# Kernel optimization log

Measured on AMD Instinct MI355X. Metric: run time of the kernel, lower is better.

Reference implementation:

```python
import jax, jax.numpy as jnp
import numpy as np

HEADS = 8
GROUPS = 32   # Group_cnt in the source
WIN = 16      # config.local_window_size


def _gn_nc(x, groups, eps):
    # group_norm on [N, C] (affine=False)
    N, C = x.shape
    xg = x.reshape(N, groups, C // groups)
    m = xg.mean(axis=2, keepdims=True)
    v = xg.var(axis=2, keepdims=True)
    return ((xg - m) / jnp.sqrt(v + eps)).reshape(N, C)


def _gn_nchw(x, groups, eps):
    # group_norm on [B, C, H, W] (affine=False)
    B, C, H, W = x.shape
    xg = x.reshape(B, groups, C // groups, H, W)
    m = xg.mean(axis=(2, 3, 4), keepdims=True)
    v = xg.var(axis=(2, 3, 4), keepdims=True)
    return ((xg - m) / jnp.sqrt(v + eps)).reshape(B, C, H, W)


def _conv3x3(x, w, b=None):
    y = jax.lax.conv_general_dilated(x, w, (1, 1), 'SAME',
                                     dimension_numbers=('NCHW', 'OIHW', 'NCHW'))
    return y if b is None else y + b[None, :, None, None]


def _forward(x, temb, conv1_w, conv1_b, conv2_w, g_diff, g_res, g2, g3,
             qkv2_w, qkv2_b, out2_w, qkv3_w, qkv3_b, out3_w,
             lsa_qkv_w, lsa_out_w):
    # ---- Residual_Block (layer1) ----
    h = _gn_nchw(x, GROUPS, 1e-6)
    h = _conv3x3(h, conv1_w, conv1_b)
    h = h + g_diff * temb[:, :, None, None]      # gate_diffusion (ReZero-style gate)
    h = jax.nn.silu(h)
    h = _gn_nchw(h, GROUPS, 1e-6)
    h = _conv3x3(h, conv2_w)
    h = _gn_nchw(h, GROUPS, 1e-6)
    x = x + g_res * h                            # gate_residual

    B, C, Fq, T = x.shape
    Dh = C // HEADS
    scale = 1.0 / jnp.sqrt(jnp.float32(Dh))      # (F/heads)**0.5 divisor

    # ---- SelfAttention over frequency axis (layer2): batch B*T, seq Fq ----
    xf = x.transpose(0, 3, 2, 1).reshape(B * T, Fq, C)
    qkv = xf @ qkv2_w + qkv2_b                   # [B*T, Fq, 3C]
    q, k, v = [t.reshape(B * T, Fq, HEADS, Dh) for t in jnp.split(qkv, 3, axis=-1)]
    p = jax.nn.softmax(jnp.einsum('bLhf,blhf->bLlh', q, k) * scale, axis=2)
    y = jnp.einsum('blhf,bLlh->bLhf', v, p).reshape(B * T, Fq, C) @ out2_w
    y = _gn_nc(y.reshape(-1, C), GROUPS, 1e-5).reshape(B * T, Fq, C)
    xf = xf + g2 * y                             # gate2

    # ---- GlobalAttention over time axis (layer3): batch B*Fq, seq T ----
    xt = xf.reshape(B, T, Fq, C).transpose(0, 2, 1, 3).reshape(B * Fq, T, C)
    qkv = xt @ qkv3_w + qkv3_b
    q, k, v = [t.reshape(B * Fq, T, HEADS, Dh) for t in jnp.split(qkv, 3, axis=-1)]
    p = jax.nn.softmax(jnp.einsum('bhf,blhf->blh', q.mean(axis=1), k) * scale, axis=1)
    y = jnp.einsum('blhf,blh->bhf', v, p).reshape(B * Fq, C) @ out3_w
    y = _gn_nc(y, GROUPS, 1e-5).reshape(B * Fq, 1, C)
    xt = xt + g3 * y                             # gate3, broadcast over T
    x = xt.reshape(B, Fq, T, C).transpose(0, 3, 1, 2)

    # ---- LSA_block (layer4): pre-norm local windowed attention along T, residual ----
    h = _gn_nchw(x, GROUPS, 1e-5)
    h = h.transpose(0, 2, 3, 1).reshape(B * Fq, T, C)
    nw = T // WIN
    qkv = (h @ lsa_qkv_w).reshape(B * Fq, nw, WIN, 3 * C)
    q, k, v = [t.reshape(B * Fq, nw, WIN, HEADS, Dh) for t in jnp.split(qkv, 3, axis=-1)]
    p = jax.nn.softmax(jnp.einsum('nwqhd,nwkhd->nwqkh', q, k) * scale, axis=3)
    o = jnp.einsum('nwqkh,nwkhd->nwqhd', p, v).reshape(B * Fq, T, C) @ lsa_out_w
    return x + o.reshape(B, Fq, T, C).transpose(0, 3, 1, 2)


def setup_inputs() -> dict:
    key = jax.random.key(0)
    ks = jax.random.split(key, 10)
    B, C, Fq, T = 4, 256, 64, 256
    w = lambda k, s: jax.random.normal(k, s, dtype=jnp.float32) * 0.02
    return {
        'x': jax.random.normal(ks[0], (B, C, Fq, T), dtype=jnp.float32),
        'temb': jax.random.normal(ks[1], (B, C), dtype=jnp.float32),
        'conv1_w': w(ks[2], (C, C, 3, 3)),
        'conv1_b': jnp.zeros((C,), jnp.float32),
        'conv2_w': w(ks[3], (C, C, 3, 3)),
        'g_diff': jnp.full((1,), 0.5, jnp.float32),
        'g_res': jnp.full((1,), 0.5, jnp.float32),
        'g2': jnp.full((1,), 0.5, jnp.float32),
        'g3': jnp.full((1,), 0.5, jnp.float32),
        'qkv2_w': w(ks[4], (C, 3 * C)),
        'qkv2_b': jnp.zeros((3 * C,), jnp.float32),
        'out2_w': w(ks[5], (C, C)),
        'qkv3_w': w(ks[6], (C, 3 * C)),
        'qkv3_b': jnp.zeros((3 * C,), jnp.float32),
        'out3_w': w(ks[7], (C, C)),
        'lsa_qkv_w': w(ks[8], (C, 3 * C)),
        'lsa_out_w': w(ks[9], (C, C)),
    }


def reference(x, temb, conv1_w, conv1_b, conv2_w, g_diff, g_res, g2, g3,
              qkv2_w, qkv2_b, out2_w, qkv3_w, qkv3_b, out3_w,
              lsa_qkv_w, lsa_out_w):
    return _forward(x, temb, conv1_w, conv1_b, conv2_w, g_diff, g_res, g2, g3,
                    qkv2_w, qkv2_b, out2_w, qkv3_w, qkv3_b, out3_w,
                    lsa_qkv_w, lsa_out_w)
```

## Files before the change

kernel.cpp:

```cpp
#include <hip/hip_runtime.h>

#define NN 16777216
#define CC 256
#define FF 64
#define TT 256

typedef short v8s __attribute__((ext_vector_type(8)));
typedef float v4f __attribute__((ext_vector_type(4)));

__device__ __forceinline__ unsigned short f2bf(float f) {
  unsigned u = __float_as_uint(f);
  u += 0x7fff + ((u >> 16) & 1);
  return (unsigned short)(u >> 16);
}
__device__ __forceinline__ float bf2f(unsigned short h) {
  return __uint_as_float(((unsigned)h) << 16);
}
__device__ __forceinline__ unsigned packbf2(float a, float b) {
  return (unsigned)f2bf(a) | ((unsigned)f2bf(b) << 16);
}
__device__ __forceinline__ void unpack8(uint4 u, float* d) {
  d[0] = __uint_as_float(u.x << 16); d[1] = __uint_as_float(u.x & 0xffff0000u);
  d[2] = __uint_as_float(u.y << 16); d[3] = __uint_as_float(u.y & 0xffff0000u);
  d[4] = __uint_as_float(u.z << 16); d[5] = __uint_as_float(u.z & 0xffff0000u);
  d[6] = __uint_as_float(u.w << 16); d[7] = __uint_as_float(u.w & 0xffff0000u);
}

__device__ __forceinline__ void blockReduce2(float& a, float& b, float* sbuf) {
  #pragma unroll
  for (int off = 32; off > 0; off >>= 1) {
    a += __shfl_down(a, off, 64);
    b += __shfl_down(b, off, 64);
  }
  int w = threadIdx.x >> 6;
  if ((threadIdx.x & 63) == 0) { sbuf[w] = a; sbuf[4 + w] = b; }
  __syncthreads();
  if (threadIdx.x == 0) {
    a = sbuf[0] + sbuf[1] + sbuf[2] + sbuf[3];
    b = sbuf[4] + sbuf[5] + sbuf[6] + sbuf[7];
  }
}

__global__ void zero_stats_k(float* p) { p[threadIdx.x] = 0.f; }

__global__ void convw_bf_k(const float* __restrict__ w, unsigned short* __restrict__ wb) {
  int s = blockIdx.x * 256 + threadIdx.x;
  if (s < 589824) {
    int co = s / 2304, r = s % 2304;
    int ci = r / 9, tap = r % 9;
    wb[(tap * 256 + co) * 256 + ci] = f2bf(w[s]);
  }
}

__global__ void matT_bf_k(const float* __restrict__ w, unsigned short* __restrict__ bt, int N, int total) {
  int s = blockIdx.x * 256 + threadIdx.x;
  if (s < total) {
    int k = s / N, n = s % N;
    bt[n * 256 + k] = f2bf(w[s]);
  }
}

__global__ __launch_bounds__(256) void gn_stats_contig(const float* __restrict__ src, float* __restrict__ stats) {
  __shared__ float sbuf[8];
  int grp = blockIdx.x >> 3, chunk = blockIdx.x & 7;
  const float4* p = (const float4*)src + grp * 32768 + chunk * 4096;
  float s = 0.f, ss = 0.f;
  for (int i = threadIdx.x; i < 4096; i += 256) {
    float4 v = p[i];
    s += v.x + v.y + v.z + v.w;
    ss += v.x * v.x + v.y * v.y + v.z * v.z + v.w * v.w;
  }
  blockReduce2(s, ss, sbuf);
  if (threadIdx.x == 0) { atomicAdd(&stats[grp], s); atomicAdd(&stats[128 + grp], ss); }
}

__global__ __launch_bounds__(256) void gn_apply_tr_k(const float* __restrict__ src,
    const float* __restrict__ stats, unsigned short* __restrict__ XC, float eps) {
  __shared__ float sT[32][33];
  int bx = blockIdx.x;
  int r = bx >> 6;
  int c0 = ((bx >> 3) & 7) * 32;
  int t0 = (bx & 7) * 32;
  int b = r >> 6, f = r & 63;
  int tl = threadIdx.x & 31, tr = threadIdx.x >> 5;
  #pragma unroll
  for (int i = 0; i < 4; ++i) {
    int c = c0 + tr + i * 8;
    int grp = b * 32 + (c >> 3);
    float mean = stats[grp] * (1.f / 131072.f);
    float var = stats[128 + grp] * (1.f / 131072.f) - mean * mean;
    float rv = rsqrtf(var + eps);
    float v = src[((b * 256 + c) * 64 + f) * 256 + t0 + tl];
    sT[tr + i * 8][tl] = (v - mean) * rv;
  }
  __syncthreads();
  #pragma unroll
  for (int i = 0; i < 4; ++i) {
    int t = t0 + tr + i * 8;
    XC[(((size_t)(b * 64 + f)) * 256 + t) * 256 + c0 + tl] = f2bf(sT[tl][tr + i * 8]);
  }
}

__global__ __launch_bounds__(256) void gn_tr_resid_k(const float* __restrict__ h,
    const float* __restrict__ x, const float* __restrict__ stats,
    const float* __restrict__ gate, float* __restrict__ XF, float eps) {
  __shared__ float sT[32][33];
  int bx = blockIdx.x;
  int r = bx >> 6;
  int c0 = ((bx >> 3) & 7) * 32;
  int t0 = (bx & 7) * 32;
  int b = r >> 6, f = r & 63;
  int tl = threadIdx.x & 31, tr = threadIdx.x >> 5;
  float g = gate[0];
  #pragma unroll
  for (int i = 0; i < 4; ++i) {
    int c = c0 + tr + i * 8;
    int grp = b * 32 + (c >> 3);
    float mean = stats[grp] * (1.f / 131072.f);
    float var = stats[128 + grp] * (1.f / 131072.f) - mean * mean;
    float rv = rsqrtf(var + eps);
    int idx = ((b * 256 + c) * 64 + f) * 256 + t0 + tl;
    sT[tr + i * 8][tl] = x[idx] + g * (h[idx] - mean) * rv;
  }
  __syncthreads();
  #pragma unroll
  for (int i = 0; i < 4; ++i) {
    int t = t0 + tr + i * 8;
    XF[(((size_t)(b * 256 + t)) * 64 + f) * 256 + c0 + tl] = sT[tl][tr + i * 8];
  }
}

__global__ __launch_bounds__(256, 2) void conv3x3_mfma_k(const unsigned short* __restrict__ XC,
    const unsigned short* __restrict__ wb, const float* __restrict__ bias,
    const float* __restrict__ temb, const float* __restrict__ gd,
    float* __restrict__ out, int mode) {
  __shared__ __align__(16) unsigned short sIn[3][258][40];
  __shared__ __align__(16) unsigned short sW[128][40];
  int f  = blockIdx.x;
  int b  = blockIdx.y >> 1;
  int co0 = (blockIdx.y & 1) * 128;
  int tid = threadIdx.x;
  int wave = tid >> 6, lane = tid & 63;
  int lm = lane & 15, quad = lane >> 4;
  int w64 = wave * 64;
  v4f acc[4][8];
  #pragma unroll
  for (int i = 0; i < 4; ++i)
    #pragma unroll
    for (int j = 0; j < 8; ++j) acc[i][j] = (v4f)(0.f);

  for (int ci0 = 0; ci0 < 256; ci0 += 32) {
    __syncthreads();
    for (int s = tid; s < 3096; s += 256) {
      int df = s / 1032, r = s - df * 1032;
      int tl = r >> 2, part = r & 3;
      int fi = f + df - 1, tg = tl - 1;
      uint4 val = make_uint4(0, 0, 0, 0);
      if (fi >= 0 && fi < 64 && tg >= 0 && tg < 256)
        val = *(const uint4*)&XC[(((size_t)(b * 64 + fi)) * 256 + tg) * 256 + ci0 + part * 8];
      *(uint4*)&sIn[df][tl][part * 8] = val;
    }
    for (int tap = 0; tap < 9; ++tap) {
      __syncthreads();
      {
        int co = tid >> 2, part = tid & 3;
        *(uint4*)&sW[co][part * 8] =
            *(const uint4*)&wb[((size_t)(tap * 256) + co0 + co) * 256 + ci0 + part * 8];
        int s1 = tid + 256;
        co = s1 >> 2; part = s1 & 3;
        *(uint4*)&sW[co][part * 8] =
            *(const uint4*)&wb[((size_t)(tap * 256) + co0 + co) * 256 + ci0 + part * 8];
      }
      __syncthreads();
      int df = tap / 3, dt = tap - df * 3;
      v8s A[4];
      #pragma unroll
      for (int mt = 0; mt < 4; ++mt)
        A[mt] = *(const v8s*)&sIn[df][w64 + mt * 16 + lm + dt][quad * 8];
      #pragma unroll
      for (int nt = 0; nt < 8; ++nt) {
        v8s B = *(const v8s*)&sW[nt * 16 + lm][quad * 8];
        #pragma unroll
        for (int mt = 0; mt < 4; ++mt)
          acc[mt][nt] = __builtin_amdgcn_mfma_f32_16x16x32_bf16(A[mt], B, acc[mt][nt], 0, 0, 0);
      }
    }
  }
  float gdv = mode ? gd[0] : 0.f;
  #pragma unroll
  for (int nt = 0; nt < 8; ++nt) {
    int co = co0 + nt * 16 + lm;
    float bb = 0.f;
    if (mode) bb = bias[co] + gdv * temb[b * 256 + co];
    #pragma unroll
    for (int mt = 0; mt < 4; ++mt) {
      int t = w64 + mt * 16 + quad * 4;
      float v0 = acc[mt][nt][0] + bb, v1 = acc[mt][nt][1] + bb;
      float v2 = acc[mt][nt][2] + bb, v3 = acc[mt][nt][3] + bb;
      if (mode) {
        v0 = v0 / (1.f + expf(-v0)); v1 = v1 / (1.f + expf(-v1));
        v2 = v2 / (1.f + expf(-v2)); v3 = v3 / (1.f + expf(-v3));
      }
      float4 o; o.x = v0; o.y = v1; o.z = v2; o.w = v3;
      *(float4*)&out[(((size_t)b * 256 + co) * 64 + f) * 256 + t] = o;
    }
  }
}

__global__ __launch_bounds__(256) void gemm_af32_k(const float* __restrict__ A, int lda,
    const unsigned short* __restrict__ BT, const float* __restrict__ bias,
    unsigned short* __restrict__ Cb, int ldc,
    const float* __restrict__ gstats, int growbase, float eps) {
  __shared__ __align__(16) unsigned short sA[128][40];
  __shared__ __align__(16) unsigned short sB[128][40];
  int n0 = blockIdx.x * 128, m0 = blockIdx.y * 128;
  int tid = threadIdx.x;
  int wave = tid >> 6, lane = tid & 63;
  int wm = wave >> 1, wn = wave & 1;
  int lm = lane & 15, quad = lane >> 4;
  v4f acc[4][4];
  #pragma unroll
  for (int i = 0; i < 4; ++i)
    #pragma unroll
    for (int j = 0; j < 4; ++j) acc[i][j] = (v4f)(0.f);

  for (int k0 = 0; k0 < 256; k0 += 32) {
    __syncthreads();
    #pragma unroll
    for (int i = 0; i < 4; ++i) {
      int s = tid + i * 256;
      int row = s >> 3, k4 = s & 7;
      float4 av = *(const float4*)&A[(size_t)(m0 + row) * lda + k0 + k4 * 4];
      if (gstats) {
        int grp = ((growbase + m0 + row) >> 14) * 32 + ((k0 + k4 * 4) >> 3);
        float mean = gstats[grp] * (1.f / 131072.f);
        float var = gstats[128 + grp] * (1.f / 131072.f) - mean * mean;
        float rr = rsqrtf(var + eps);
        av.x = (av.x - mean) * rr; av.y = (av.y - mean) * rr;
        av.z = (av.z - mean) * rr; av.w = (av.w - mean) * rr;
      }
      *(uint2*)&sA[row][k4 * 4] = make_uint2(packbf2(av.x, av.y), packbf2(av.z, av.w));
    }
    #pragma unroll
    for (int i = 0; i < 2; ++i) {
      int s = tid + i * 256;
      int n = s >> 2, part = s & 3;
      *(uint4*)&sB[n][part * 8] = *(const uint4*)&BT[(size_t)(n0 + n) * 256 + k0 + part * 8];
    }
    __syncthreads();
    v8s Af[4];
    #pragma unroll
    for (int mt = 0; mt < 4; ++mt)
      Af[mt] = *(const v8s*)&sA[wm * 64 + mt * 16 + lm][quad * 8];
    #pragma unroll
    for (int nt = 0; nt < 4; ++nt) {
      v8s Bf = *(const v8s*)&sB[wn * 64 + nt * 16 + lm][quad * 8];
      #pragma unroll
      for (int mt = 0; mt < 4; ++mt)
        acc[mt][nt] = __builtin_amdgcn_mfma_f32_16x16x32_bf16(Af[mt], Bf, acc[mt][nt], 0, 0, 0);
    }
  }
  #pragma unroll
  for (int nt = 0; nt < 4; ++nt) {
    int col = n0 + wn * 64 + nt * 16 + lm;
    float bb = bias ? bias[col] : 0.f;
    #pragma unroll
    for (int mt = 0; mt < 4; ++mt) {
      int row = m0 + wm * 64 + mt * 16 + quad * 4;
      #pragma unroll
      for (int r = 0; r < 4; ++r)
        Cb[(size_t)(row + r) * ldc + col] = f2bf(acc[mt][nt][r] + bb);
    }
  }
}

__global__ __launch_bounds__(256) void gemm_abf16_k(const unsigned short* __restrict__ A, int lda,
    const unsigned short* __restrict__ BT, float* __restrict__ xf,
    unsigned short* __restrict__ Cb, int ldc, const float* __restrict__ gate) {
  __shared__ __align__(16) unsigned short sA[128][40];
  __shared__ __align__(16) unsigned short sB[128][40];
  int n0 = blockIdx.x * 128, m0 = blockIdx.y * 128;
  int tid = threadIdx.x;
  int wave = tid >> 6, lane = tid & 63;
  int wm = wave >> 1, wn = wave & 1;
  int lm = lane & 15, quad = lane >> 4;
  v4f acc[4][4];
  #pragma unroll
  for (int i = 0; i < 4; ++i)
    #pragma unroll
    for (int j = 0; j < 4; ++j) acc[i][j] = (v4f)(0.f);

  for (int k0 = 0; k0 < 256; k0 += 32) {
    __syncthreads();
    #pragma unroll
    for (int i = 0; i < 2; ++i) {
      int s = tid + i * 256;
      int row = s >> 2, part = s & 3;
      *(uint4*)&sA[row][part * 8] = *(const uint4*)&A[(size_t)(m0 + row) * lda + k0 + part * 8];
      *(uint4*)&sB[row][part * 8] = *(const uint4*)&BT[(size_t)(n0 + row) * 256 + k0 + part * 8];
    }
    __syncthreads();
    v8s Af[4];
    #pragma unroll
    for (int mt = 0; mt < 4; ++mt)
      Af[mt] = *(const v8s*)&sA[wm * 64 + mt * 16 + lm][quad * 8];
    #pragma unroll
    for (int nt = 0; nt < 4; ++nt) {
      v8s Bf = *(const v8s*)&sB[wn * 64 + nt * 16 + lm][quad * 8];
      #pragma unroll
      for (int mt = 0; mt < 4; ++mt)
        acc[mt][nt] = __builtin_amdgcn_mfma_f32_16x16x32_bf16(Af[mt], Bf, acc[mt][nt], 0, 0, 0);
    }
  }
  if (xf) {
    float g = gate[0];
    #pragma unroll
    for (int mt = 0; mt < 4; ++mt) {
      int rowb = m0 + wm * 64 + mt * 16 + quad * 4;
      #pragma unroll
      for (int r = 0; r < 4; ++r) {
        #pragma unroll
        for (int nt = 0; nt < 4; ++nt) {
          float v = acc[mt][nt][r];
          float s = v, q = v * v;
          s += __shfl_xor(s, 1); q += __shfl_xor(q, 1);
          s += __shfl_xor(s, 2); q += __shfl_xor(q, 2);
          s += __shfl_xor(s, 4); q += __shfl_xor(q, 4);
          float m = s * 0.125f;
          float var = q * 0.125f - m * m;
          float norm = (v - m) * rsqrtf(var + 1e-5f);
          int col = n0 + wn * 64 + nt * 16 + lm;
          size_t idx = (size_t)(rowb + r) * 256 + col;
          xf[idx] += g * norm;
        }
      }
    }
  } else {
    #pragma unroll
    for (int nt = 0; nt < 4; ++nt) {
      int col = n0 + wn * 64 + nt * 16 + lm;
      #pragma unroll
      for (int mt = 0; mt < 4; ++mt) {
        int row = m0 + wm * 64 + mt * 16 + quad * 4;
        #pragma unroll
        for (int r = 0; r < 4; ++r)
          Cb[(size_t)(row + r) * ldc + col] = f2bf(acc[mt][nt][r]);
      }
    }
  }
}

__global__ __launch_bounds__(256) void gemm_k(const float* __restrict__ A, int lda,
    const float* __restrict__ Bm, int N, const float* __restrict__ bias,
    float* __restrict__ Cm, int ldc) {
  __shared__ __align__(16) float sA[16][64];
  __shared__ __align__(16) float sB[16][64];
  int n0 = blockIdx.x * 64, m0 = blockIdx.y * 64;
  int tid = threadIdx.x;
  int tx = tid & 15, ty = tid >> 4;
  int arow = m0 + (tid >> 2), acol = (tid & 3) * 4;
  int brow = tid >> 4, bcol = (tid & 15) * 4;
  float acc[4][4] = {};
  for (int k0 = 0; k0 < 256; k0 += 16) {
    __syncthreads();
    float4 av = *(const float4*)&A[(size_t)arow * lda + k0 + acol];
    sA[acol + 0][tid >> 2] = av.x;
    sA[acol + 1][tid >> 2] = av.y;
    sA[acol + 2][tid >> 2] = av.z;
    sA[acol + 3][tid >> 2] = av.w;
    *(float4*)&sB[brow][bcol] = *(const float4*)&Bm[(k0 + brow) * N + n0 + bcol];
    __syncthreads();
    #pragma unroll
    for (int kk = 0; kk < 16; ++kk) {
      float4 a = *(const float4*)&sA[kk][ty * 4];
      float4 b = *(const float4*)&sB[kk][tx * 4];
      float aa[4] = {a.x, a.y, a.z, a.w};
      float bb[4] = {b.x, b.y, b.z, b.w};
      #pragma unroll
      for (int i = 0; i < 4; ++i)
        #pragma unroll
        for (int j = 0; j < 4; ++j)
          acc[i][j] += aa[i] * bb[j];
    }
  }
  #pragma unroll
  for (int i = 0; i < 4; ++i)
    #pragma unroll
    for (int j = 0; j < 4; ++j) {
      int n = n0 + tx * 4 + j;
      float v = acc[i][j];
      if (bias) v += bias[n];
      Cm[(size_t)(m0 + ty * 4 + i) * ldc + n] = v;
    }
}

__global__ __launch_bounds__(256) void xf_to_xt_k(const float* __restrict__ XF, float* __restrict__ XT) {
  int rowid = blockIdx.x * 4 + (threadIdx.x >> 6);
  int lane = threadIdx.x & 63;
  int b = rowid >> 14, f = (rowid >> 8) & 63, t = rowid & 255;
  int src = ((b * TT + t) * FF + f) * CC + lane * 4;
  int dst = rowid * CC + lane * 4;
  *(float4*)&XT[dst] = *(const float4*)&XF[src];
}

__global__ __launch_bounds__(256) void final_out_k(const float* __restrict__ XT,
    const unsigned short* __restrict__ O2b, float* __restrict__ out, int rbase) {
  __shared__ float sT[32][33];
  int bx = blockIdx.x;
  int rl = bx >> 6;
  int t0 = ((bx >> 3) & 7) * 32;
  int c0 = (bx & 7) * 32;
  int rg = rbase + rl;
  int b = rg >> 6, f = rg & 63;
  int tc = threadIdx.x & 31, tr = threadIdx.x >> 5;
  #pragma unroll
  for (int i = 0; i < 4; ++i) {
    int t = t0 + tr + i * 8;
    sT[tr + i * 8][tc] = XT[(size_t)rg * 65536 + t * 256 + c0 + tc]
                       + bf2f(O2b[(size_t)rl * 65536 + t * 256 + c0 + tc]);
  }
  __syncthreads();
  #pragma unroll
  for (int i = 0; i < 4; ++i) {
    int c = c0 + tr + i * 8;
    out[((b * CC + c) * FF + f) * TT + t0 + tc] = sT[tc][tr + i * 8];
  }
}

__global__ __launch_bounds__(256) void attn2_mfma_k(unsigned short* __restrict__ Q) {
  __shared__ __align__(16) unsigned short sP[4][64][72];
  __shared__ __align__(16) unsigned short sVt[4][32][72];
  int bt = blockIdx.x;
  int tid = threadIdx.x;
  int wave = tid >> 6, lane = tid & 63;
  int lm = lane & 15, quad = lane >> 4;
  const float scale = 0.17677669529663687f;
  size_t rowbase = (size_t)bt * 64;
  unsigned short (*P)[72] = sP[wave];
  unsigned short (*Vt)[72] = sVt[wave];
  #pragma unroll
  for (int hh = 0; hh < 2; ++hh) {
    int h = wave * 2 + hh;
    int hoff = h * 32;
    v8s Af[4], Bf[4];
    #pragma unroll
    for (int mt = 0; mt < 4; ++mt)
      Af[mt] = *(const v8s*)&Q[(rowbase + mt * 16 + lm) * 768 + hoff + quad * 8];
    #pragma unroll
    for (int nt = 0; nt < 4; ++nt)
      Bf[nt] = *(const v8s*)&Q[(rowbase + nt * 16 + lm) * 768 + 256 + hoff + quad * 8];
    v4f S[4][4];
    #pragma unroll
    for (int mt = 0; mt < 4; ++mt)
      #pragma unroll
      for (int nt = 0; nt < 4; ++nt)
        S[mt][nt] = __builtin_amdgcn_mfma_f32_16x16x32_bf16(Af[mt], Bf[nt], (v4f)(0.f), 0, 0, 0);
    #pragma unroll
    for (int part = 0; part < 4; ++part) {
      uint4 u = *(const uint4*)&Q[(rowbase + lane) * 768 + 512 + hoff + part * 8];
      unsigned short* up = (unsigned short*)&u;
      #pragma unroll
      for (int j = 0; j < 8; ++j) Vt[part * 8 + j][lane] = up[j];
    }
    float inv[4][4];
    #pragma unroll
    for (int mt = 0; mt < 4; ++mt) {
      #pragma unroll
      for (int r = 0; r < 4; ++r) {
        float v0 = S[mt][0][r] * scale, v1 = S[mt][1][r] * scale;
        float v2 = S[mt][2][r] * scale, v3 = S[mt][3][r] * scale;
        float mx = fmaxf(fmaxf(v0, v1), fmaxf(v2, v3));
        mx = fmaxf(mx, __shfl_xor(mx, 1));
        mx = fmaxf(mx, __shfl_xor(mx, 2));
        mx = fmaxf(mx, __shfl_xor(mx, 4));
        mx = fmaxf(mx, __shfl_xor(mx, 8));
        float e0 = __expf(v0 - mx), e1 = __expf(v1 - mx);
        float e2 = __expf(v2 - mx), e3 = __expf(v3 - mx);
        float sm = e0 + e1 + e2 + e3;
        sm += __shfl_xor(sm, 1);
        sm += __shfl_xor(sm, 2);
        sm += __shfl_xor(sm, 4);
        sm += __shfl_xor(sm, 8);
        inv[mt][r] = 1.f / sm;
        int row = mt * 16 + quad * 4 + r;
        P[row][lm]      = f2bf(e0);
        P[row][16 + lm] = f2bf(e1);
        P[row][32 + lm] = f2bf(e2);
        P[row][48 + lm] = f2bf(e3);
      }
    }
    v8s Ap[4][2], Bv[2][2];
    #pragma unroll
    for (int mt = 0; mt < 4; ++mt)
      #pragma unroll
      for (int kc = 0; kc < 2; ++kc)
        Ap[mt][kc] = *(const v8s*)&P[mt * 16 + lm][kc * 32 + quad * 8];
    #pragma unroll
    for (int nd = 0; nd < 2; ++nd)
      #pragma unroll
      for (int kc = 0; kc < 2; ++kc)
        Bv[nd][kc] = *(const v8s*)&Vt[nd * 16 + lm][kc * 32 + quad * 8];
    #pragma unroll
    for (int mt = 0; mt < 4; ++mt) {
      #pragma unroll
      for (int nd = 0; nd < 2; ++nd) {
        v4f O = (v4f)(0.f);
        O = __builtin_amdgcn_mfma_f32_16x16x32_bf16(Ap[mt][0], Bv[nd][0], O, 0, 0, 0);
        O = __builtin_amdgcn_mfma_f32_16x16x32_bf16(Ap[mt][1], Bv[nd][1], O, 0, 0, 0);
        #pragma unroll
        for (int r = 0; r < 4; ++r)
          P[mt * 16 + quad * 4 + r][nd * 16 + lm] = f2bf(O[r] * inv[mt][r]);
      }
    }
    #pragma unroll
    for (int part = 0; part < 4; ++part) {
      uint4 u = *(const uint4*)&P[lane][part * 8];
      *(uint4*)&Q[(rowbase + lane) * 768 + hoff + part * 8] = u;
    }
  }
}

__global__ __launch_bounds__(256) void attn3_k(const unsigned short* __restrict__ Q3,
                                               float* __restrict__ y3, int bf_base) {
  __shared__ float part[8][32];
  __shared__ float sqm[32];
  __shared__ float sp[256];
  __shared__ float sred[256];
  int bfl = blockIdx.x >> 3, h = blockIdx.x & 7;
  int tid = threadIdx.x;
  int tg = tid >> 5, d = tid & 31;
  const float scale = 0.17677669529663687f;
  int rowbase = bfl * 256;
  float s = 0.f;
  for (int t = tg * 32; t < tg * 32 + 32; ++t) s += bf2f(Q3[(size_t)(rowbase + t) * 768 + h * 32 + d]);
  part[tg][d] = s;
  __syncthreads();
  if (tid < 32) {
    float m = 0.f;
    for (int g = 0; g < 8; ++g) m += part[g][tid];
    sqm[tid] = m * (1.f / 256.f);
  }
  __syncthreads();
  {
    float dot = 0.f;
    const unsigned short* kp = &Q3[(size_t)(rowbase + tid) * 768 + 256 + h * 32];
    for (int dd = 0; dd < 32; ++dd) dot += sqm[dd] * bf2f(kp[dd]);
    sp[tid] = dot * scale;
    sred[tid] = sp[tid];
  }
  __syncthreads();
  for (int st = 128; st > 0; st >>= 1) { if (tid < st) sred[tid] = fmaxf(sred[tid], sred[tid + st]); __syncthreads(); }
  float mx = sred[0];
  __syncthreads();
  float e = expf(sp[tid] - mx);
  sred[tid] = e;
  __syncthreads();
  for (int st = 128; st > 0; st >>= 1) { if (tid < st) sred[tid] += sred[tid + st]; __syncthreads(); }
  float rinv = 1.f / sred[0];
  sp[tid] = e * rinv;
  __syncthreads();
  float acc = 0.f;
  for (int t = tg * 32; t < tg * 32 + 32; ++t)
    acc += sp[t] * bf2f(Q3[(size_t)(rowbase + t) * 768 + 512 + h * 32 + d]);
  part[tg][d] = acc;
  __syncthreads();
  if (tid < 32) {
    float o = 0.f;
    for (int g = 0; g < 8; ++g) o += part[g][tid];
    y3[(size_t)(bf_base + bfl) * 256 + h * 32 + tid] = o;
  }
}

__global__ __launch_bounds__(256) void lsa_attn_k(unsigned short* __restrict__ Q4) {
  __shared__ __align__(16) float sX[16][772];
  __shared__ float sS[8][16][17];
  __shared__ float sInv[8][16];
  int bfl = blockIdx.x >> 4, w = blockIdx.x & 15;
  int tid = threadIdx.x;
  size_t rb = ((size_t)(bfl * 256 + w * 16)) * 768;
  for (int s = tid; s < 1536; s += 256) {
    int t = s / 96, c8 = (s - t * 96) * 8;
    unpack8(*(const uint4*)&Q4[rb + t * 768 + c8], &sX[t][c8]);
  }
  __syncthreads();
  const float scale = 0.17677669529663687f;
  #pragma unroll
  for (int rep = 0; rep < 8; ++rep) {
    int idx = tid + rep * 256;
    int h = idx >> 8, q = (idx >> 4) & 15, k = idx & 15;
    float dot = 0.f;
    const float* qp = &sX[q][h * 32];
    const float* kp = &sX[k][256 + h * 32];
    for (int d = 0; d < 32; ++d) dot += qp[d] * kp[d];
    sS[h][q][k] = dot * scale;
  }
  __syncthreads();
  if (tid < 128) {
    int h = tid >> 4, q = tid & 15;
    float mx = -1e30f;
    for (int k = 0; k < 16; ++k) mx = fmaxf(mx, sS[h][q][k]);
    float sum = 0.f;
    for (int k = 0; k < 16; ++k) { float e = expf(sS[h][q][k] - mx); sS[h][q][k] = e; sum += e; }
    sInv[h][q] = 1.f / sum;
  }
  __syncthreads();
  #pragma unroll
  for (int rep = 0; rep < 8; ++rep) {
    int idx = tid + rep * 256;
    int t = idx >> 7, c2 = (idx & 127) * 2;
    int h = c2 >> 5;
    float a0 = 0.f, a1 = 0.f;
    for (int k = 0; k < 16; ++k) {
      float p = sS[h][t][k];
      a0 += p * sX[k][512 + c2];
      a1 += p * sX[k][512 + c2 + 1];
    }
    float riv = sInv[h][t];
    *(unsigned*)&Q4[rb + t * 768 + c2] = packbf2(a0 * riv, a1 * riv);
  }
}

__global__ void gn_rows_k(const float* __restrict__ src, float* __restrict__ dst, int total) {
  int s = blockIdx.x * 256 + threadIdx.x;
  if (s >= total) return;
  int base = s * 8;
  float4 a = *(const float4*)&src[base];
  float4 b = *(const float4*)&src[base + 4];
  float m = (a.x + a.y + a.z + a.w + b.x + b.y + b.z + b.w) * 0.125f;
  float q = (a.x * a.x + a.y * a.y + a.z * a.z + a.w * a.w +
             b.x * b.x + b.y * b.y + b.z * b.z + b.w * b.w) * 0.125f - m * m;
  float r = rsqrtf(q + 1e-5f);
  a.x = (a.x - m) * r; a.y = (a.y - m) * r; a.z = (a.z - m) * r; a.w = (a.w - m) * r;
  b.x = (b.x - m) * r; b.y = (b.y - m) * r; b.z = (b.z - m) * r; b.w = (b.w - m) * r;
  *(float4*)&dst[base] = a;
  *(float4*)&dst[base + 4] = b;
}

__global__ __launch_bounds__(256) void bcast_add_k(float* __restrict__ XT, const float* __restrict__ y3n,
                                                   const float* __restrict__ gate) {
  int i4 = blockIdx.x * 256 + threadIdx.x;
  int flat = i4 * 4;
  int r = flat >> 16, c = flat & 255;
  float g = gate[0];
  float4 v = ((float4*)XT)[i4];
  float4 a = *(const float4*)&y3n[r * 256 + c];
  v.x += g * a.x; v.y += g * a.y; v.z += g * a.z; v.w += g * a.w;
  ((float4*)XT)[i4] = v;
}

__global__ __launch_bounds__(256) void gn_stats_xt_k(const float* __restrict__ X, float* __restrict__ stats) {
  __shared__ float sbuf[8];
  int bx = blockIdx.x;
  int b = bx >> 11, g = (bx >> 6) & 31, f = bx & 63;
  size_t base = (size_t)(b * 64 + f) * 65536 + g * 8;
  float s = 0.f, ss = 0.f;
  for (int i = threadIdx.x; i < 2048; i += 256) {
    int t = i >> 3, c = i & 7;
    float v = X[base + t * 256 + c];
    s += v; ss += v * v;
  }
  blockReduce2(s, ss, sbuf);
  if (threadIdx.x == 0) { atomicAdd(&stats[b * 32 + g], s); atomicAdd(&stats[128 + b * 32 + g], ss); }
}

extern "C" void kernel_launch(void* const* d_in, const int* in_sizes, int n_in,
                              void* d_out, int out_size, void* d_ws, size_t ws_size,
                              hipStream_t stream) {
  (void)in_sizes; (void)n_in; (void)out_size;
  const float* x        = (const float*)d_in[0];
  const float* temb     = (const float*)d_in[1];
  const float* conv1_w  = (const float*)d_in[2];
  const float* conv1_b  = (const float*)d_in[3];
  const float* conv2_w  = (const float*)d_in[4];
  const float* g_diff   = (const float*)d_in[5];
  const float* g_res    = (const float*)d_in[6];
  const float* g2       = (const float*)d_in[7];
  const float* g3       = (const float*)d_in[8];
  const float* qkv2_w   = (const float*)d_in[9];
  const float* qkv2_b   = (const float*)d_in[10];
  const float* out2_w   = (const float*)d_in[11];
  const float* qkv3_w   = (const float*)d_in[12];
  const float* qkv3_b   = (const float*)d_in[13];
  const float* out3_w   = (const float*)d_in[14];
  const float* lsa_qkv_w = (const float*)d_in[15];
  const float* lsa_out_w = (const float*)d_in[16];
  float* out = (float*)d_out;
  float* ws = (float*)d_ws;

  int NCHv = 4;
  {
    auto need = [](int nch) -> size_t {
      size_t rows = 65536 / nch;
      size_t uslots = rows * 512;
      if (uslots < 8388608) uslots = 8388608;
      return 4ull * ((size_t)NN + uslots + 950272 + 196864 + 256);
    };
    if (ws_size >= need(1)) NCHv = 1;
    else if (ws_size >= need(2)) NCHv = 2;
  }
  const size_t rows = 65536 / NCHv;

  float* W = ws;
  float* U = ws + (size_t)NN;
  unsigned short* XC  = (unsigned short*)U;
  unsigned short* QB  = (unsigned short*)U;
  unsigned short* O2B = (unsigned short*)(U + rows * 384);
  size_t uslots = rows * 512; if (uslots < 8388608) uslots = 8388608;
  float* WREG = U + uslots;
  unsigned short* WB1   = (unsigned short*)WREG;
  unsigned short* WB2   = WB1 + 589824;
  unsigned short* QKV2T = WB2 + 589824;
  unsigned short* OUT2T = QKV2T + 196608;
  unsigned short* QKV3T = OUT2T + 65536;
  unsigned short* LSAQT = QKV3T + 196608;
  unsigned short* LSAOT = LSAQT + 196608;
  float* Y3    = WREG + 950272;
  float* Y3O   = Y3 + 65536;
  float* Y3N   = Y3O + 65536;
  float* STATS = Y3N + 65536;
  float* D = out;

  dim3 b256(256);
  convw_bf_k<<<2304, b256, 0, stream>>>(conv1_w, WB1);
  convw_bf_k<<<2304, b256, 0, stream>>>(conv2_w, WB2);
  matT_bf_k<<<768, b256, 0, stream>>>(qkv2_w, QKV2T, 768, 196608);
  matT_bf_k<<<256, b256, 0, stream>>>(out2_w, OUT2T, 256, 65536);
  matT_bf_k<<<768, b256, 0, stream>>>(qkv3_w, QKV3T, 768, 196608);
  matT_bf_k<<<768, b256, 0, stream>>>(lsa_qkv_w, LSAQT, 768, 196608);
  matT_bf_k<<<256, b256, 0, stream>>>(lsa_out_w, LSAOT, 256, 65536);

  zero_stats_k<<<1, b256, 0, stream>>>(STATS);
  gn_stats_contig<<<1024, b256, 0, stream>>>(x, STATS);
  gn_apply_tr_k<<<16384, b256, 0, stream>>>(x, STATS, XC, 1e-6f);
  conv3x3_mfma_k<<<dim3(64, 8), b256, 0, stream>>>(XC, WB1, conv1_b, temb, g_diff, W, 1);
  zero_stats_k<<<1, b256, 0, stream>>>(STATS);
  gn_stats_contig<<<1024, b256, 0, stream>>>(W, STATS);
  gn_apply_tr_k<<<16384, b256, 0, stream>>>(W, STATS, XC, 1e-6f);
  conv3x3_mfma_k<<<dim3(64, 8), b256, 0, stream>>>(XC, WB2, nullptr, nullptr, nullptr, W, 0);
  zero_stats_k<<<1, b256, 0, stream>>>(STATS);
  gn_stats_contig<<<1024, b256, 0, stream>>>(W, STATS);
  gn_tr_resid_k<<<16384, b256, 0, stream>>>(W, x, STATS, g_res, D, 1e-6f);

  for (int c = 0; c < NCHv; ++c) {
    float* XFr = D + (size_t)c * rows * 256;
    gemm_af32_k<<<dim3(6, rows / 128), b256, 0, stream>>>(XFr, 256, QKV2T, qkv2_b, QB, 768, nullptr, 0, 0.f);
    attn2_mfma_k<<<rows / 64, b256, 0, stream>>>(QB);
    gemm_abf16_k<<<dim3(2, rows / 128), b256, 0, stream>>>(QB, 768, OUT2T, XFr, nullptr, 256, g2);
  }

  xf_to_xt_k<<<16384, b256, 0, stream>>>(D, W);
  for (int c = 0; c < NCHv; ++c) {
    const float* XTr = W + (size_t)c * rows * 256;
    gemm_af32_k<<<dim3(6, rows / 128), b256, 0, stream>>>(XTr, 256, QKV3T, qkv3_b, QB, 768, nullptr, 0, 0.f);
    attn3_k<<<(rows / 256) * 8, b256, 0, stream>>>(QB, Y3, c * (int)(rows / 256));
  }
  gemm_k<<<dim3(4, 4), b256, 0, stream>>>(Y3, 256, out3_w, 256, nullptr, Y3O, 256);
  gn_rows_k<<<32, b256, 0, stream>>>(Y3O, Y3N, 8192);
  bcast_add_k<<<16384, b256, 0, stream>>>(W, Y3N, g3);

  zero_stats_k<<<1, b256, 0, stream>>>(STATS);
  gn_stats_xt_k<<<8192, b256, 0, stream>>>(W, STATS);
  for (int c = 0; c < NCHv; ++c) {
    const float* XTr = W + (size_t)c * rows * 256;
    gemm_af32_k<<<dim3(6, rows / 128), b256, 0, stream>>>(XTr, 256, LSAQT, nullptr, QB, 768,
                                                          STATS, (int)(c * rows), 1e-5f);
    lsa_attn_k<<<(rows / 256) * 16, b256, 0, stream>>>(QB);
    gemm_abf16_k<<<dim3(2, rows / 128), b256, 0, stream>>>(QB, 768, LSAOT, nullptr, O2B, 256, nullptr);
    final_out_k<<<(rows / 256) * 64, b256, 0, stream>>>(W, O2B, out, c * (int)(rows / 256));
  }
}
```

Measured before the change: 1.116 ms.

## Fuse GroupNorm stats into conv epilogue, merge prep kernels, vectorize attn3

Several independent changes. All weight-conversion kernels and the stats zeroing are merged into one prep launch, and each GroupNorm gets its own stats slot. The two conv kernels now accumulate per-group sums and sums of squares in their epilogue, which removes two full passes that re-read the 64 MB activation just to compute statistics. The conv main loop now stages input one frequency row at a time together with three weight taps, cutting barriers and shrinking the input tile in shared memory. attn3 loads bf16 data with 16-byte vector loads and reduces over more partial rows. The costs are extra epilogue work and atomics in the conv, and a layout change to its shared-memory staging.

After: 1.095 ms. About the same (-1.9%).

```diff
diff --git a/kernel.cpp b/kernel.cpp
--- a/kernel.cpp
+++ b/kernel.cpp
@@ -41,23 +41,39 @@
   }
 }
 
-__global__ void zero_stats_k(float* p) { p[threadIdx.x] = 0.f; }
-
-__global__ void convw_bf_k(const float* __restrict__ w, unsigned short* __restrict__ wb) {
-  int s = blockIdx.x * 256 + threadIdx.x;
+__global__ void prep_all_k(const float* __restrict__ c1w, const float* __restrict__ c2w,
+    const float* __restrict__ q2w, const float* __restrict__ o2w, const float* __restrict__ q3w,
+    const float* __restrict__ lqw, const float* __restrict__ low,
+    unsigned short* __restrict__ WB1, unsigned short* __restrict__ WB2,
+    unsigned short* __restrict__ Q2T, unsigned short* __restrict__ O2T,
+    unsigned short* __restrict__ Q3T, unsigned short* __restrict__ LQT,
+    unsigned short* __restrict__ LOT, float* __restrict__ stats) {
+  long s = (long)blockIdx.x * 256 + threadIdx.x;
+  if (s < 1024) { stats[s] = 0.f; return; }
+  s -= 1024;
   if (s < 589824) {
-    int co = s / 2304, r = s % 2304;
+    int co = (int)(s / 2304), r = (int)(s % 2304);
     int ci = r / 9, tap = r % 9;
-    wb[(tap * 256 + co) * 256 + ci] = f2bf(w[s]);
-  }
-}
-
-__global__ void matT_bf_k(const float* __restrict__ w, unsigned short* __restrict__ bt, int N, int total) {
-  int s = blockIdx.x * 256 + threadIdx.x;
-  if (s < total) {
-    int k = s / N, n = s % N;
-    bt[n * 256 + k] = f2bf(w[s]);
-  }
+    WB1[(tap * 256 + co) * 256 + ci] = f2bf(c1w[s]);
+    return;
+  }
+  s -= 589824;
+  if (s < 589824) {
+    int co = (int)(s / 2304), r = (int)(s % 2304);
+    int ci = r / 9, tap = r % 9;
+    WB2[(tap * 256 + co) * 256 + ci] = f2bf(c2w[s]);
+    return;
+  }
+  s -= 589824;
+  if (s < 196608) { int k = (int)(s / 768), n = (int)(s % 768); Q2T[n * 256 + k] = f2bf(q2w[s]); return; }
+  s -= 196608;
+  if (s < 65536)  { int k = (int)(s / 256), n = (int)(s % 256); O2T[n * 256 + k] = f2bf(o2w[s]); return; }
+  s -= 65536;
+  if (s < 196608) { int k = (int)(s / 768), n = (int)(s % 768); Q3T[n * 256 + k] = f2bf(q3w[s]); return; }
+  s -= 196608;
+  if (s < 196608) { int k = (int)(s / 768), n = (int)(s % 768); LQT[n * 256 + k] = f2bf(lqw[s]); return; }
+  s -= 196608;
+  if (s < 65536)  { int k = (int)(s / 256), n = (int)(s % 256); LOT[n * 256 + k] = f2bf(low[s]); return; }
 }
 
 __global__ __launch_bounds__(256) void gn_stats_contig(const float* __restrict__ src, float* __restrict__ stats) {
@@ -133,9 +149,9 @@
 __global__ __launch_bounds__(256, 2) void conv3x3_mfma_k(const unsigned short* __restrict__ XC,
     const unsigned short* __restrict__ wb, const float* __restrict__ bias,
     const float* __restrict__ temb, const float* __restrict__ gd,
-    float* __restrict__ out, int mode) {
-  __shared__ __align__(16) unsigned short sIn[3][258][40];
-  __shared__ __align__(16) unsigned short sW[128][40];
+    float* __restrict__ out, float* __restrict__ ostats, int mode) {
+  __shared__ __align__(16) unsigned short sIn[258][40];
+  __shared__ __align__(16) unsigned short sW[3][128][40];
   int f  = blockIdx.x;
   int b  = blockIdx.y >> 1;
   int co0 = (blockIdx.y & 1) * 128;
@@ -150,48 +166,49 @@
     for (int j = 0; j < 8; ++j) acc[i][j] = (v4f)(0.f);
 
   for (int ci0 = 0; ci0 < 256; ci0 += 32) {
-    __syncthreads();
-    for (int s = tid; s < 3096; s += 256) {
-      int df = s / 1032, r = s - df * 1032;
-      int tl = r >> 2, part = r & 3;
-      int fi = f + df - 1, tg = tl - 1;
-      uint4 val = make_uint4(0, 0, 0, 0);
-      if (fi >= 0 && fi < 64 && tg >= 0 && tg < 256)
-        val = *(const uint4*)&XC[(((size_t)(b * 64 + fi)) * 256 + tg) * 256 + ci0 + part * 8];
-      *(uint4*)&sIn[df][tl][part * 8] = val;
-    }
-    for (int tap = 0; tap < 9; ++tap) {
+    for (int df = 0; df < 3; ++df) {
       __syncthreads();
-      {
-        int co = tid >> 2, part = tid & 3;
-        *(uint4*)&sW[co][part * 8] =
-            *(const uint4*)&wb[((size_t)(tap * 256) + co0 + co) * 256 + ci0 + part * 8];
-        int s1 = tid + 256;
-        co = s1 >> 2; part = s1 & 3;
-        *(uint4*)&sW[co][part * 8] =
-            *(const uint4*)&wb[((size_t)(tap * 256) + co0 + co) * 256 + ci0 + part * 8];
+      for (int s = tid; s < 1032; s += 256) {
+        int tl = s >> 2, part = s & 3;
+        int fi = f + df - 1, tg = tl - 1;
+        uint4 val = make_uint4(0, 0, 0, 0);
+        if (fi >= 0 && fi < 64 && tg >= 0 && tg < 256)
+          val = *(const uint4*)&XC[(((size_t)(b * 64 + fi)) * 256 + tg) * 256 + ci0 + part * 8];
+        *(uint4*)&sIn[tl][part * 8] = val;
+      }
+      for (int s = tid; s < 1536; s += 256) {
+        int tap3 = s >> 9, r = s & 511;
+        int co = r >> 2, part = r & 3;
+        *(uint4*)&sW[tap3][co][part * 8] =
+            *(const uint4*)&wb[((size_t)((df * 3 + tap3) * 256) + co0 + co) * 256 + ci0 + part * 8];
       }
       __syncthreads();
-      int df = tap / 3, dt = tap - df * 3;
-      v8s A[4];
-      #pragma unroll
-      for (int mt = 0; mt < 4; ++mt)
-        A[mt] = *(const v8s*)&sIn[df][w64 + mt * 16 + lm + dt][quad * 8];
-      #pragma unroll
-      for (int nt = 0; nt < 8; ++nt) {
-        v8s B = *(const v8s*)&sW[nt * 16 + lm][quad * 8];
+      #pragma unroll
+      for (int dt = 0; dt < 3; ++dt) {
+        v8s A[4];
         #pragma unroll
         for (int mt = 0; mt < 4; ++mt)
-          acc[mt][nt] = __builtin_amdgcn_mfma_f32_16x16x32_bf16(A[mt], B, acc[mt][nt], 0, 0, 0);
+          A[mt] = *(const v8s*)&sIn[w64 + mt * 16 + lm + dt][quad * 8];
+        #pragma unroll
+        for (int nt = 0; nt < 8; ++nt) {
+          v8s B = *(const v8s*)&sW[dt][nt * 16 + lm][quad * 8];
+          #pragma unroll
+          for (int mt = 0; mt < 4; ++mt)
+            acc[mt][nt] = __builtin_amdgcn_mfma_f32_16x16x32_bf16(A[mt], B, acc[mt][nt], 0, 0, 0);
+        }
       }
     }
   }
+  __syncthreads();
+  float* sStat = (float*)sIn;
   float gdv = mode ? gd[0] : 0.f;
+  float sch, qch;
   #pragma unroll
   for (int nt = 0; nt < 8; ++nt) {
     int co = co0 + nt * 16 + lm;
     float bb = 0.f;
     if (mode) bb = bias[co] + gdv * temb[b * 256 + co];
+    sch = 0.f; qch = 0.f;
     #pragma unroll
     for (int mt = 0; mt < 4; ++mt) {
       int t = w64 + mt * 16 + quad * 4;
@@ -203,6 +220,33 @@
       }
       float4 o; o.x = v0; o.y = v1; o.z = v2; o.w = v3;
       *(float4*)&out[(((size_t)b * 256 + co) * 64 + f) * 256 + t] = o;
+      sch += v0 + v1 + v2 + v3;
+      qch += v0 * v0 + v1 * v1 + v2 * v2 + v3 * v3;
+    }
+    sch += __shfl_xor(sch, 16); qch += __shfl_xor(qch, 16);
+    sch += __shfl_xor(sch, 32); qch += __shfl_xor(qch, 32);
+    if (quad == 0) {
+      sStat[((wave * 8 + nt) * 16 + lm) * 2]     = sch;
+      sStat[((wave * 8 + nt) * 16 + lm) * 2 + 1] = qch;
+    }
+  }
+  __syncthreads();
+  if (tid < 128) {
+    int c = tid;
+    int nt = c >> 4, lmm = c & 15;
+    float s = 0.f, q = 0.f;
+    #pragma unroll
+    for (int w = 0; w < 4; ++w) {
+      s += sStat[((w * 8 + nt) * 16 + lmm) * 2];
+      q += sStat[((w * 8 + nt) * 16 + lmm) * 2 + 1];
+    }
+    s += __shfl_xor(s, 1); q += __shfl_xor(q, 1);
+    s += __shfl_xor(s, 2); q += __shfl_xor(q, 2);
+    s += __shfl_xor(s, 4); q += __shfl_xor(q, 4);
+    if ((c & 7) == 0) {
+      int g = (co0 + c) >> 3;
+      atomicAdd(&ostats[b * 32 + g], s);
+      atomicAdd(&ostats[128 + b * 32 + g], q);
     }
   }
 }
@@ -522,29 +566,45 @@
 
 __global__ __launch_bounds__(256) void attn3_k(const unsigned short* __restrict__ Q3,
                                                float* __restrict__ y3, int bf_base) {
-  __shared__ float part[8][32];
+  __shared__ float sQp[64][33];
   __shared__ float sqm[32];
   __shared__ float sp[256];
   __shared__ float sred[256];
   int bfl = blockIdx.x >> 3, h = blockIdx.x & 7;
   int tid = threadIdx.x;
-  int tg = tid >> 5, d = tid & 31;
+  int tq = tid >> 2, c4 = tid & 3;
+  int d8 = c4 * 8;
   const float scale = 0.17677669529663687f;
-  int rowbase = bfl * 256;
-  float s = 0.f;
-  for (int t = tg * 32; t < tg * 32 + 32; ++t) s += bf2f(Q3[(size_t)(rowbase + t) * 768 + h * 32 + d]);
-  part[tg][d] = s;
+  size_t rowbase = (size_t)bfl * 256;
+  {
+    float a[8] = {};
+    #pragma unroll
+    for (int i = 0; i < 4; ++i) {
+      int t = i * 64 + tq;
+      float v[8];
+      unpack8(*(const uint4*)&Q3[(rowbase + t) * 768 + h * 32 + d8], v);
+      #pragma unroll
+      for (int j = 0; j < 8; ++j) a[j] += v[j];
+    }
+    #pragma unroll
+    for (int j = 0; j < 8; ++j) sQp[tq][d8 + j] = a[j];
+  }
   __syncthreads();
   if (tid < 32) {
     float m = 0.f;
-    for (int g = 0; g < 8; ++g) m += part[g][tid];
+    for (int g = 0; g < 64; ++g) m += sQp[g][tid];
     sqm[tid] = m * (1.f / 256.f);
   }
   __syncthreads();
   {
     float dot = 0.f;
-    const unsigned short* kp = &Q3[(size_t)(rowbase + tid) * 768 + 256 + h * 32];
-    for (int dd = 0; dd < 32; ++dd) dot += sqm[dd] * bf2f(kp[dd]);
+    #pragma unroll
+    for (int p = 0; p < 4; ++p) {
+      float v[8];
+      unpack8(*(const uint4*)&Q3[(rowbase + tid) * 768 + 256 + h * 32 + p * 8], v);
+      #pragma unroll
+      for (int j = 0; j < 8; ++j) dot += sqm[p * 8 + j] * v[j];
+    }
     sp[tid] = dot * scale;
     sred[tid] = sp[tid];
   }
@@ -559,14 +619,24 @@
   float rinv = 1.f / sred[0];
   sp[tid] = e * rinv;
   __syncthreads();
-  float acc = 0.f;
-  for (int t = tg * 32; t < tg * 32 + 32; ++t)
-    acc += sp[t] * bf2f(Q3[(size_t)(rowbase + t) * 768 + 512 + h * 32 + d]);
-  part[tg][d] = acc;
+  {
+    float a[8] = {};
+    #pragma unroll
+    for (int i = 0; i < 4; ++i) {
+      int t = i * 64 + tq;
+      float w = sp[t];
+      float v[8];
+      unpack8(*(const uint4*)&Q3[(rowbase + t) * 768 + 512 + h * 32 + d8], v);
+      #pragma unroll
+      for (int j = 0; j < 8; ++j) a[j] += w * v[j];
+    }
+    #pragma unroll
+    for (int j = 0; j < 8; ++j) sQp[tq][d8 + j] = a[j];
+  }
   __syncthreads();
   if (tid < 32) {
     float o = 0.f;
-    for (int g = 0; g < 8; ++g) o += part[g][tid];
+    for (int g = 0; g < 64; ++g) o += sQp[g][tid];
     y3[(size_t)(bf_base + bfl) * 256 + h * 32 + tid] = o;
   }
 }
@@ -693,7 +763,7 @@
       size_t rows = 65536 / nch;
       size_t uslots = rows * 512;
       if (uslots < 8388608) uslots = 8388608;
-      return 4ull * ((size_t)NN + uslots + 950272 + 196864 + 256);
+      return 4ull * ((size_t)NN + uslots + 950272 + 198000);
     };
     if (ws_size >= need(1)) NCHv = 1;
     else if (ws_size >= need(2)) NCHv = 2;
@@ -718,28 +788,20 @@
   float* Y3O   = Y3 + 65536;
   float* Y3N   = Y3O + 65536;
   float* STATS = Y3N + 65536;
+  float* ST0 = STATS, *ST1 = STATS + 256, *ST2 = STATS + 512, *ST3 = STATS + 768;
   float* D = out;
 
   dim3 b256(256);
-  convw_bf_k<<<2304, b256, 0, stream>>>(conv1_w, WB1);
-  convw_bf_k<<<2304, b256, 0, stream>>>(conv2_w, WB2);
-  matT_bf_k<<<768, b256, 0, stream>>>(qkv2_w, QKV2T, 768, 196608);
-  matT_bf_k<<<256, b256, 0, stream>>>(out2_w, OUT2T, 256, 65536);
-  matT_bf_k<<<768, b256, 0, stream>>>(qkv3_w, QKV3T, 768, 196608);
-  matT_bf_k<<<768, b256, 0, stream>>>(lsa_qkv_w, LSAQT, 768, 196608);
-  matT_bf_k<<<256, b256, 0, stream>>>(lsa_out_w, LSAOT, 256, 65536);
-
-  zero_stats_k<<<1, b256, 0, stream>>>(STATS);
-  gn_stats_contig<<<1024, b256, 0, stream>>>(x, STATS);
-  gn_apply_tr_k<<<16384, b256, 0, stream>>>(x, STATS, XC, 1e-6f);
-  conv3x3_mfma_k<<<dim3(64, 8), b256, 0, stream>>>(XC, WB1, conv1_b, temb, g_diff, W, 1);
-  zero_stats_k<<<1, b256, 0, stream>>>(STATS);
-  gn_stats_contig<<<1024, b256, 0, stream>>>(W, STATS);
-  gn_apply_tr_k<<<16384, b256, 0, stream>>>(W, STATS, XC, 1e-6f);
-  conv3x3_mfma_k<<<dim3(64, 8), b256, 0, stream>>>(XC, WB2, nullptr, nullptr, nullptr, W, 0);
-  zero_stats_k<<<1, b256, 0, stream>>>(STATS);
-  gn_stats_contig<<<1024, b256, 0, stream>>>(W, STATS);
-  gn_tr_resid_k<<<16384, b256, 0, stream>>>(W, x, STATS, g_res, D, 1e-6f);
+  prep_all_k<<<7428, b256, 0, stream>>>(conv1_w, conv2_w, qkv2_w, out2_w, qkv3_w,
+                                        lsa_qkv_w, lsa_out_w,
+                                        WB1, WB2, QKV2T, OUT2T, QKV3T, LSAQT, LSAOT, STATS);
+
+  gn_stats_contig<<<1024, b256, 0, stream>>>(x, ST0);
+  gn_apply_tr_k<<<16384, b256, 0, stream>>>(x, ST0, XC, 1e-6f);
+  conv3x3_mfma_k<<<dim3(64, 8), b256, 0, stream>>>(XC, WB1, conv1_b, temb, g_diff, W, ST1, 1);
+  gn_apply_tr_k<<<16384, b256, 0, stream>>>(W, ST1, XC, 1e-6f);
+  conv3x3_mfma_k<<<dim3(64, 8), b256, 0, stream>>>(XC, WB2, nullptr, nullptr, nullptr, W, ST2, 0);
+  gn_tr_resid_k<<<16384, b256, 0, stream>>>(W, x, ST2, g_res, D, 1e-6f);
 
   for (int c = 0; c < NCHv; ++c) {
     float* XFr = D + (size_t)c * rows * 256;
@@ -758,12 +820,11 @@
   gn_rows_k<<<32, b256, 0, stream>>>(Y3O, Y3N, 8192);
   bcast_add_k<<<16384, b256, 0, stream>>>(W, Y3N, g3);
 
-  zero_stats_k<<<1, b256, 0, stream>>>(STATS);
-  gn_stats_xt_k<<<8192, b256, 0, stream>>>(W, STATS);
+  gn_stats_xt_k<<<8192, b256, 0, stream>>>(W, ST3);
   for (int c = 0; c < NCHv; ++c) {
     const float* XTr = W + (size_t)c * rows * 256;
     gemm_af32_k<<<dim3(6, rows / 128), b256, 0, stream>>>(XTr, 256, LSAQT, nullptr, QB, 768,
-                                                          STATS, (int)(c * rows), 1e-5f);
+                                                          ST3, (int)(c * rows), 1e-5f);
     lsa_attn_k<<<(rows / 256) * 16, b256, 0, stream>>>(QB);
     gemm_abf16_k<<<dim3(2, rows / 128), b256, 0, stream>>>(QB, 768, LSAOT, nullptr, O2B, 256, nullptr);
     final_out_k<<<(rows / 256) * 64, b256, 0, stream>>>(W, O2B, out, c * (int)(rows / 256));
```
